# Optimization experiments

Hardware: AMD Instinct MI355X
Metric: run time of the kernel (lower is better)

## Reference

```python
import jax, jax.numpy as jnp
import numpy as np

NUM_BITS = 8
VMIN, VMAX = 0.0, 1.0
THRESH = 4.0
K_SYN = 32


def gray_code_encode(x):
    # (batch, features) -> (batch, features*NUM_BITS) binary float bits
    norm = (jnp.clip(x, VMIN, VMAX) - VMIN) / (VMAX - VMIN)
    levels = jnp.round(norm * (2 ** NUM_BITS - 1)).astype(jnp.int32)
    gray = levels ^ (levels >> 1)
    bit_pos = jnp.arange(NUM_BITS, dtype=jnp.int32)
    bits = ((gray[..., None] >> bit_pos) & 1).astype(jnp.float32)
    return bits.reshape(x.shape[0], -1)


def _make_sparse_weight(key, n_neurons, prev_size):
    # k random synapses per neuron with +/-1 weights (rest zero), as in
    # _initialise_layer_weights (standard, non-dynamic path)
    kc, ks = jax.random.split(key)
    cols = jax.random.randint(kc, (n_neurons, K_SYN), 0, prev_size)
    signs = jax.random.randint(ks, (n_neurons, K_SYN), 0, 2).astype(jnp.float32) * 2 - 1
    rows = jnp.broadcast_to(jnp.arange(n_neurons)[:, None], (n_neurons, K_SYN))
    return jnp.zeros((n_neurons, prev_size), jnp.float32).at[rows, cols].set(signs)


def setup_inputs() -> dict:
    key = jax.random.key(0)
    kx, k0, k1, k2, ko = jax.random.split(key, 5)
    batch, feat = 512, 256
    hidden, classes, n_hidden_layers = 4096, 1000, 3
    enc = feat * NUM_BITS  # 2048
    x = jax.random.uniform(kx, (batch, feat), dtype=jnp.float32)
    W0 = _make_sparse_weight(k0, hidden, enc)
    W1 = _make_sparse_weight(k1, hidden, hidden)
    W2 = _make_sparse_weight(k2, hidden, hidden)
    out_w = jax.random.normal(ko, (n_hidden_layers, hidden, classes), dtype=jnp.float32) * 0.01
    return {"x": x, "W0": W0, "W1": W1, "W2": W2, "out_w": out_w}


def reference(x, W0, W1, W2, out_w):
    prev = gray_code_encode(x)  # (b, enc)
    out = jnp.zeros((x.shape[0], out_w.shape[-1]), jnp.float32)
    for i, W in enumerate((W0, W1, W2)):
        z = prev @ W.T                                  # (b, hidden)
        prev = (z >= THRESH).astype(jnp.float32)        # binary activation
        out = out + prev @ out_w[i]                     # accumulate per-layer
    return out
```

## Files before the change

### kernel.cpp

```cpp
#include <hip/hip_runtime.h>
#include <stdint.h>

typedef unsigned long long u64;
typedef __attribute__((ext_vector_type(8))) short bf16x8;
typedef __attribute__((ext_vector_type(4))) float f32x4;
typedef __attribute__((ext_vector_type(4))) unsigned u32x4;

#define BATCH 512
#define FEAT 256
#define ENC 2048
#define HID 4096
#define CLS 1000
#define KTOT 12288
#define NSPLIT 16
#define KSPLIT 768
#define PARTLD 1024

#define OFF_ENC2   0
#define OFF_ACT2   131072
#define OFF_TABLE  917504
#define OFF_COUNTS 1703936
#define OFF_WT     1753088
#define OFF_PART   26918912
#define PART_BYTES (16ull * 512 * 1024 * 4)
#define WS_NEED    (OFF_PART + PART_BYTES)

static __device__ inline unsigned short f2bf(float f) {
    unsigned u = __float_as_uint(f);
    return (unsigned short)((u + 0x7FFFu + ((u >> 16) & 1u)) >> 16);
}

static __device__ inline void gld16(const void* g, void* s) {
    __builtin_amdgcn_global_load_lds((const __attribute__((address_space(1))) void*)g,
                                     (__attribute__((address_space(3))) void*)s, 16, 0, 0);
}

__global__ void __launch_bounds__(256)
k_prep(const float* __restrict__ x, u64* __restrict__ enc2,
       const float* __restrict__ W0, const float* __restrict__ W1,
       const float* __restrict__ W2,
       uint16_t* __restrict__ table, int* __restrict__ counts,
       const float* __restrict__ out_w, short* __restrict__ wt) {
    __shared__ short tile[64 * 68];
    __shared__ int cnt4[4];
    int bid = blockIdx.x;
    int t = threadIdx.x;
    int lane = t & 63;
    int wv = t >> 6;

    if (bid < 512) {
        int wid = bid * 4 + wv;
        int f = wid >> 3, bg = wid & 7;
        float v = x[(size_t)(bg * 64 + lane) * FEAT + f];
        v = fminf(fmaxf(v, 0.0f), 1.0f);
        int lev = (int)rintf(v * 255.0f);
        unsigned gray = (unsigned)(lev ^ (lev >> 1));
        u64 w = 0;
        #pragma unroll
        for (int bit = 0; bit < 8; ++bit) {
            u64 m = __ballot((gray >> bit) & 1u);
            if (lane == bit) w = m;
        }
        if (lane < 8) enc2[(size_t)bg * ENC + f * 8 + lane] = w;
        return;
    }
    if (bid < 5632) {
        if (t < 4) cnt4[t] = 0;
        __syncthreads();
        int wsid = (bid - 512) * 4 + wv;
        int row, base, cidx;
        if (wsid < HID) { row = wsid; base = 0; cidx = wv; }
        else {
            int w2 = wsid - HID;
            row = HID + (w2 >> 1);
            base = (w2 & 1) * 2048;
            cidx = wv >> 1;
        }
        const float* Wr;
        if (row < HID)          Wr = W0 + (size_t)row * ENC;
        else if (row < 2 * HID) Wr = W1 + (size_t)(row - HID) * HID + base;
        else                    Wr = W2 + (size_t)(row - 2 * HID) * HID + base;
        const u32x4* p4 = (const u32x4*)Wr;
        u32x4 v[8];
        #pragma unroll
        for (int j = 0; j < 8; ++j) v[j] = __builtin_nontemporal_load(p4 + j * 64 + lane);
        uint16_t* te = table + (size_t)row * 32;
        #pragma unroll
        for (int j = 0; j < 8; ++j) {
            unsigned a0 = v[j].x, a1 = v[j].y, a2 = v[j].z, a3 = v[j].w;
            if (a0 | a1 | a2 | a3) {
                int col0 = base + j * 256 + lane * 4;
                if (a0) { int s = atomicAdd(&cnt4[cidx], 1);
                          te[s] = (uint16_t)((unsigned)col0       | ((a0 >> 16) & 0x8000u)); }
                if (a1) { int s = atomicAdd(&cnt4[cidx], 1);
                          te[s] = (uint16_t)((unsigned)(col0 + 1) | ((a1 >> 16) & 0x8000u)); }
                if (a2) { int s = atomicAdd(&cnt4[cidx], 1);
                          te[s] = (uint16_t)((unsigned)(col0 + 2) | ((a2 >> 16) & 0x8000u)); }
                if (a3) { int s = atomicAdd(&cnt4[cidx], 1);
                          te[s] = (uint16_t)((unsigned)(col0 + 3) | ((a3 >> 16) & 0x8000u)); }
            }
        }
        __syncthreads();
        if (lane == 0) counts[row] = cnt4[cidx];
        return;
    }
    {
        int b2 = bid - 5632;
        int kt = b2 % 192, ct = b2 / 192;
        int k0 = kt * 64, c0 = ct * 64;
        {
            int rrow = t >> 4, c4 = t & 15;
            int c = c0 + c4 * 4;
            #pragma unroll
            for (int rd = 0; rd < 4; ++rd) {
                int kl = rd * 16 + rrow;
                f32x4 vv;
                if (c < CLS)
                    vv = __builtin_nontemporal_load(
                        (const f32x4*)&out_w[(size_t)(k0 + kl) * CLS + c]);
                else { vv.x = 0.0f; vv.y = 0.0f; vv.z = 0.0f; vv.w = 0.0f; }
                short* d = &tile[kl * 68 + c4 * 4];
                d[0] = (short)f2bf(vv.x); d[1] = (short)f2bf(vv.y);
                d[2] = (short)f2bf(vv.z); d[3] = (short)f2bf(vv.w);
            }
        }
        __syncthreads();
        {
            int chunk = t & 7, cl2 = t >> 3;
            #pragma unroll
            for (int rd = 0; rd < 2; ++rd) {
                int c_local = rd * 32 + cl2;
                int c = c0 + c_local;
                unsigned s8[8];
                #pragma unroll
                for (int j = 0; j < 8; ++j)
                    s8[j] = (unsigned)(unsigned short)tile[(chunk * 8 + j) * 68 + c_local];
                uint4 pk;
                pk.x = s8[0] | (s8[1] << 16);
                pk.y = s8[2] | (s8[3] << 16);
                pk.z = s8[4] | (s8[5] << 16);
                pk.w = s8[6] | (s8[7] << 16);
                *(uint4*)&wt[(size_t)c * KTOT + k0 + ((chunk ^ (c & 7)) * 8)] = pk;
            }
        }
    }
}

__global__ void k_layer(const u64* __restrict__ prev2, int Kstride,
                        const uint16_t* __restrict__ table_l, const int* __restrict__ counts_l,
                        u64* __restrict__ actout) {
    int wid = __builtin_amdgcn_readfirstlane(blockIdx.x * 4 + (threadIdx.x >> 6));
    int lane = threadIdx.x & 63;
    int n = wid >> 3, bg = wid & 7;
    const u64* prow = prev2 + (size_t)bg * Kstride;
    const uint4* tq = (const uint4*)(table_l + (size_t)n * 32);
    int cnt = counts_l[n];
    int z = 0;
    #pragma unroll
    for (int q = 0; q < 4; ++q) {
        uint4 e4 = tq[q];
        unsigned es[4] = {e4.x, e4.y, e4.z, e4.w};
        #pragma unroll
        for (int h = 0; h < 4; ++h) {
            #pragma unroll
            for (int s2 = 0; s2 < 2; ++s2) {
                int e = q * 8 + h * 2 + s2;
                if (e < cnt) {
                    unsigned ent = (es[h] >> (s2 * 16)) & 0xFFFFu;
                    u64 w = prow[ent & 0x7FFFu];
                    int bit = (int)((w >> lane) & 1ull);
                    z += (ent & 0x8000u) ? -bit : bit;
                }
            }
        }
    }
    u64 res = __ballot(z >= 4);
    if (lane == 0) actout[(size_t)bg * HID + n] = res;
}

template<int MODE>
__global__ void __launch_bounds__(256)
k_gemm(const u64* __restrict__ act2, const short* __restrict__ wt,
       float* __restrict__ out, float* __restrict__ part) {
    __shared__ __attribute__((aligned(16))) short As[128 * 64];
    __shared__ __attribute__((aligned(16))) short Bs[128 * 64];
    int bid = blockIdx.x;
    int mt = bid & 3, nt = (bid >> 2) & 7, ks = bid >> 5;
    int tid = threadIdx.x, lane = tid & 63;
    int wv = tid >> 6, waveM = wv & 1, waveN = wv >> 1;
    int quad = lane >> 4, cl = lane & 15;
    f32x4 acc[4][4] = {};
    const char* Bb = (const char*)(wt + (size_t)nt * 128 * KTOT + ks * KSPLIT);
    int r = tid >> 3, sub = tid & 7;
    for (int kk = 0; kk < KSPLIT; kk += 64) {
        #pragma unroll
        for (int rd = 0; rd < 4; ++rd) {
            size_t go = (size_t)(r + rd * 32) * (KTOT * 2) + kk * 2 + sub * 16;
            gld16(Bb + go, &Bs[(tid + rd * 256) * 8]);
        }
        {
            int kabs = ks * KSPLIT + kk;
            int l = kabs >> 12, nk = kabs & 4095;
            #pragma unroll
            for (int i = 0; i < 4; ++i) {
                int item = i * 256 + tid;
                int rr = item >> 3, g = item & 7;
                const u64* w8 = act2 + ((size_t)(l * 8 + mt * 2 + (rr >> 6))) * HID + nk + g * 8;
                int bl = rr & 63;
                unsigned sh[8];
                #pragma unroll
                for (int j = 0; j < 8; ++j)
                    sh[j] = (unsigned)((w8[j] >> bl) & 1ull) * 0x3F80u;
                uint4 pk;
                pk.x = sh[0] | (sh[1] << 16);
                pk.y = sh[2] | (sh[3] << 16);
                pk.z = sh[4] | (sh[5] << 16);
                pk.w = sh[6] | (sh[7] << 16);
                *(uint4*)&As[rr * 64 + ((g ^ (rr & 7)) * 8)] = pk;
            }
        }
        __syncthreads();
        #pragma unroll
        for (int s = 0; s < 2; ++s) {
            int xr = ((s * 4 + quad) ^ (cl & 7)) * 8;
            bf16x8 af[4], bfr[4];
            #pragma unroll
            for (int mf = 0; mf < 4; ++mf)
                af[mf] = *(const bf16x8*)&As[(waveM * 64 + mf * 16 + cl) * 64 + xr];
            #pragma unroll
            for (int nf = 0; nf < 4; ++nf)
                bfr[nf] = *(const bf16x8*)&Bs[(waveN * 64 + nf * 16 + cl) * 64 + xr];
            #pragma unroll
            for (int mf = 0; mf < 4; ++mf)
                #pragma unroll
                for (int nf = 0; nf < 4; ++nf)
                    acc[mf][nf] = __builtin_amdgcn_mfma_f32_16x16x32_bf16(
                        af[mf], bfr[nf], acc[mf][nf], 0, 0, 0);
        }
        __syncthreads();
    }
    if (MODE == 0) {
        float* pbase = part + (size_t)ks * (BATCH * PARTLD);
        #pragma unroll
        for (int mf = 0; mf < 4; ++mf)
            #pragma unroll
            for (int nf = 0; nf < 4; ++nf) {
                int cp = nt * 128 + waveN * 64 + nf * 16 + cl;
                #pragma unroll
                for (int rr = 0; rr < 4; ++rr) {
                    int mg = mt * 128 + waveM * 64 + mf * 16 + quad * 4 + rr;
                    pbase[(size_t)mg * PARTLD + cp] = acc[mf][nf][rr];
                }
            }
    } else {
        #pragma unroll
        for (int mf = 0; mf < 4; ++mf)
            #pragma unroll
            for (int nf = 0; nf < 4; ++nf) {
                int cp = nt * 128 + waveN * 64 + nf * 16 + cl;
                if (cp < CLS) {
                    #pragma unroll
                    for (int rr = 0; rr < 4; ++rr) {
                        int mg = mt * 128 + waveM * 64 + mf * 16 + quad * 4 + rr;
                        atomicAdd(&out[(size_t)mg * CLS + cp], acc[mf][nf][rr]);
                    }
                }
            }
    }
}

__global__ void k_reduce(const float* __restrict__ part, float* __restrict__ out) {
    int idx = blockIdx.x * blockDim.x + threadIdx.x;
    if (idx >= BATCH * CLS) return;
    int b = idx / CLS, c = idx - b * CLS;
    float s = 0.0f;
    #pragma unroll
    for (int sp = 0; sp < NSPLIT; ++sp)
        s += part[((size_t)sp * BATCH + b) * PARTLD + c];
    out[idx] = s;
}

extern "C" void kernel_launch(void* const* d_in, const int* in_sizes, int n_in,
                              void* d_out, int out_size, void* d_ws, size_t ws_size,
                              hipStream_t stream) {
    const float* x     = (const float*)d_in[0];
    const float* W0    = (const float*)d_in[1];
    const float* W1    = (const float*)d_in[2];
    const float* W2    = (const float*)d_in[3];
    const float* out_w = (const float*)d_in[4];
    float* out = (float*)d_out;
    char* ws = (char*)d_ws;

    u64*      enc2   = (u64*)(ws + OFF_ENC2);
    u64*      act2   = (u64*)(ws + OFF_ACT2);
    uint16_t* table  = (uint16_t*)(ws + OFF_TABLE);
    int*      counts = (int*)(ws + OFF_COUNTS);
    short*    wt     = (short*)(ws + OFF_WT);
    float*    part   = (float*)(ws + OFF_PART);

    int use_part = (ws_size >= (size_t)WS_NEED) ? 1 : 0;

    hipLaunchKernelGGL(k_prep, dim3(8704), dim3(256), 0, stream,
                       x, enc2, W0, W1, W2, table, counts, out_w, wt);
    if (!use_part)
        (void)hipMemsetAsync(d_out, 0, (size_t)BATCH * CLS * sizeof(float), stream);

    hipLaunchKernelGGL(k_layer, dim3(8192), dim3(256), 0, stream,
                       enc2, ENC, table, counts, act2);
    hipLaunchKernelGGL(k_layer, dim3(8192), dim3(256), 0, stream,
                       act2, HID, table + (size_t)HID * 32, counts + HID, act2 + 8 * HID);
    hipLaunchKernelGGL(k_layer, dim3(8192), dim3(256), 0, stream,
                       act2 + 8 * HID, HID, table + (size_t)2 * HID * 32, counts + 2 * HID,
                       act2 + 16 * HID);
    if (use_part) {
        hipLaunchKernelGGL((k_gemm<0>), dim3(512), dim3(256), 0, stream,
                           act2, wt, out, part);
        hipLaunchKernelGGL(k_reduce, dim3((BATCH * CLS + 255) / 256), dim3(256), 0, stream,
                           part, out);
    } else {
        hipLaunchKernelGGL((k_gemm<1>), dim3(512), dim3(256), 0, stream,
                           act2, wt, out, part);
    }
}
```

Baseline: 299.3 us.

## Batch four neurons per wave, remap GEMM blocks per XCD, vectorize reduce

The sparse layer kernel now has each wave compute four neurons instead of one, cutting the grid by four and amortizing per-wave setup and the prev-row base. The GEMM block index is remapped so blocks sharing an N tile and K split land on the same XCD, which should improve L2 reuse of the weight tile. The split-K reduce now reads and writes float4 vectors. The trade-off is less parallelism per layer launch and more registers per wave.

Result: no change. 303.1 us (+1.3%).

```diff
diff --git a/kernel.cpp b/kernel.cpp
--- a/kernel.cpp
+++ b/kernel.cpp
@@ -151,31 +151,40 @@
                         u64* __restrict__ actout) {
     int wid = __builtin_amdgcn_readfirstlane(blockIdx.x * 4 + (threadIdx.x >> 6));
     int lane = threadIdx.x & 63;
-    int n = wid >> 3, bg = wid & 7;
+    int bg = wid & 7, ng = wid >> 3;
     const u64* prow = prev2 + (size_t)bg * Kstride;
-    const uint4* tq = (const uint4*)(table_l + (size_t)n * 32);
-    int cnt = counts_l[n];
-    int z = 0;
+    int z[4];
     #pragma unroll
-    for (int q = 0; q < 4; ++q) {
-        uint4 e4 = tq[q];
-        unsigned es[4] = {e4.x, e4.y, e4.z, e4.w};
-        #pragma unroll
-        for (int h = 0; h < 4; ++h) {
-            #pragma unroll
-            for (int s2 = 0; s2 < 2; ++s2) {
-                int e = q * 8 + h * 2 + s2;
-                if (e < cnt) {
-                    unsigned ent = (es[h] >> (s2 * 16)) & 0xFFFFu;
-                    u64 w = prow[ent & 0x7FFFu];
-                    int bit = (int)((w >> lane) & 1ull);
-                    z += (ent & 0x8000u) ? -bit : bit;
+    for (int v = 0; v < 4; ++v) {
+        int n = ng * 4 + v;
+        const uint4* tq = (const uint4*)(table_l + (size_t)n * 32);
+        int cnt = counts_l[n];
+        int zz = 0;
+        #pragma unroll
+        for (int q = 0; q < 4; ++q) {
+            uint4 e4 = tq[q];
+            unsigned es[4] = {e4.x, e4.y, e4.z, e4.w};
+            #pragma unroll
+            for (int h = 0; h < 4; ++h) {
+                #pragma unroll
+                for (int s2 = 0; s2 < 2; ++s2) {
+                    int e = q * 8 + h * 2 + s2;
+                    if (e < cnt) {
+                        unsigned ent = (es[h] >> (s2 * 16)) & 0xFFFFu;
+                        u64 w = prow[ent & 0x7FFFu];
+                        int bit = (int)((w >> lane) & 1ull);
+                        zz += (ent & 0x8000u) ? -bit : bit;
+                    }
                 }
             }
         }
-    }
-    u64 res = __ballot(z >= 4);
-    if (lane == 0) actout[(size_t)bg * HID + n] = res;
+        z[v] = zz;
+    }
+    #pragma unroll
+    for (int v = 0; v < 4; ++v) {
+        u64 res = __ballot(z[v] >= 4);
+        if (lane == 0) actout[(size_t)bg * HID + ng * 4 + v] = res;
+    }
 }
 
 template<int MODE>
@@ -185,7 +194,11 @@
     __shared__ __attribute__((aligned(16))) short As[128 * 64];
     __shared__ __attribute__((aligned(16))) short Bs[128 * 64];
     int bid = blockIdx.x;
-    int mt = bid & 3, nt = (bid >> 2) & 7, ks = bid >> 5;
+    int xcd = bid & 7;
+    int slot = bid >> 3;
+    int mt = slot >> 4;
+    int g = ((slot & 15) << 3) | xcd;
+    int nt = g >> 4, ks = g & 15;
     int tid = threadIdx.x, lane = tid & 63;
     int wv = tid >> 6, waveM = wv & 1, waveN = wv >> 1;
     int quad = lane >> 4, cl = lane & 15;
@@ -204,8 +217,8 @@
             #pragma unroll
             for (int i = 0; i < 4; ++i) {
                 int item = i * 256 + tid;
-                int rr = item >> 3, g = item & 7;
-                const u64* w8 = act2 + ((size_t)(l * 8 + mt * 2 + (rr >> 6))) * HID + nk + g * 8;
+                int rr = item >> 3, gg = item & 7;
+                const u64* w8 = act2 + ((size_t)(l * 8 + mt * 2 + (rr >> 6))) * HID + nk + gg * 8;
                 int bl = rr & 63;
                 unsigned sh[8];
                 #pragma unroll
@@ -216,7 +229,7 @@
                 pk.y = sh[2] | (sh[3] << 16);
                 pk.z = sh[4] | (sh[5] << 16);
                 pk.w = sh[6] | (sh[7] << 16);
-                *(uint4*)&As[rr * 64 + ((g ^ (rr & 7)) * 8)] = pk;
+                *(uint4*)&As[rr * 64 + ((gg ^ (rr & 7)) * 8)] = pk;
             }
         }
         __syncthreads();
@@ -271,13 +284,15 @@
 
 __global__ void k_reduce(const float* __restrict__ part, float* __restrict__ out) {
     int idx = blockIdx.x * blockDim.x + threadIdx.x;
-    if (idx >= BATCH * CLS) return;
-    int b = idx / CLS, c = idx - b * CLS;
-    float s = 0.0f;
+    if (idx >= BATCH * (CLS / 4)) return;
+    int b = idx / (CLS / 4), c4 = idx - b * (CLS / 4);
+    f32x4 s = {0.f, 0.f, 0.f, 0.f};
     #pragma unroll
-    for (int sp = 0; sp < NSPLIT; ++sp)
-        s += part[((size_t)sp * BATCH + b) * PARTLD + c];
-    out[idx] = s;
+    for (int sp = 0; sp < NSPLIT; ++sp) {
+        f32x4 v = *(const f32x4*)&part[((size_t)sp * BATCH + b) * PARTLD + c4 * 4];
+        s.x += v.x; s.y += v.y; s.z += v.z; s.w += v.w;
+    }
+    *(f32x4*)&out[(size_t)b * CLS + c4 * 4] = s;
 }
 
 extern "C" void kernel_launch(void* const* d_in, const int* in_sizes, int n_in,
@@ -305,18 +320,18 @@
     if (!use_part)
         (void)hipMemsetAsync(d_out, 0, (size_t)BATCH * CLS * sizeof(float), stream);
 
-    hipLaunchKernelGGL(k_layer, dim3(8192), dim3(256), 0, stream,
+    hipLaunchKernelGGL(k_layer, dim3(2048), dim3(256), 0, stream,
                        enc2, ENC, table, counts, act2);
-    hipLaunchKernelGGL(k_layer, dim3(8192), dim3(256), 0, stream,
+    hipLaunchKernelGGL(k_layer, dim3(2048), dim3(256), 0, stream,
                        act2, HID, table + (size_t)HID * 32, counts + HID, act2 + 8 * HID);
-    hipLaunchKernelGGL(k_layer, dim3(8192), dim3(256), 0, stream,
+    hipLaunchKernelGGL(k_layer, dim3(2048), dim3(256), 0, stream,
                        act2 + 8 * HID, HID, table + (size_t)2 * HID * 32, counts + 2 * HID,
                        act2 + 16 * HID);
     if (use_part) {
         hipLaunchKernelGGL((k_gemm<0>), dim3(512), dim3(256), 0, stream,
                            act2, wt, out, part);
-        hipLaunchKernelGGL(k_reduce, dim3((BATCH * CLS + 255) / 256), dim3(256), 0, stream,
-                           part, out);
+        hipLaunchKernelGGL(k_reduce, dim3((BATCH * (CLS / 4) + 255) / 256), dim3(256), 0,
+                           stream, part, out);
     } else {
         hipLaunchKernelGGL((k_gemm<1>), dim3(512), dim3(256), 0, stream,
                            act2, wt, out, part);
```
